# Performance work log

Measured on AMD Instinct MI355X. Metric: run time of the kernel, lower is better.

The kernel has to match this reference:

```python
import jax, jax.numpy as jnp
import numpy as np

EMBD = 256
HEAD = 4
HD = EMBD // HEAD  # 64
EPS = 1e-5


def setup_inputs() -> dict:
    key = jax.random.key(0)
    ks = jax.random.split(key, 12)
    s = lambda fan_in: 1.0 / np.sqrt(fan_in)
    return {
        "x": jax.random.normal(ks[0], (16, 1024, EMBD), dtype=jnp.float32),
        # attention params (stored as [in, out])
        "qkv_w": jax.random.uniform(ks[1], (EMBD, 3 * EMBD), jnp.float32, -s(EMBD), s(EMBD)),
        "qkv_b": jax.random.uniform(ks[2], (3 * EMBD,), jnp.float32, -s(EMBD), s(EMBD)),
        "out_w": jax.random.uniform(ks[3], (EMBD, EMBD), jnp.float32, -s(EMBD), s(EMBD)),
        "out_b": jax.random.uniform(ks[4], (EMBD,), jnp.float32, -s(EMBD), s(EMBD)),
        # MLP params
        "fc_w": jax.random.uniform(ks[5], (EMBD, 4 * EMBD), jnp.float32, -s(EMBD), s(EMBD)),
        "fc_b": jax.random.uniform(ks[6], (4 * EMBD,), jnp.float32, -s(EMBD), s(EMBD)),
        "proj_w": jax.random.uniform(ks[7], (4 * EMBD, EMBD), jnp.float32, -s(4 * EMBD), s(4 * EMBD)),
        "proj_b": jax.random.uniform(ks[8], (EMBD,), jnp.float32, -s(4 * EMBD), s(4 * EMBD)),
        # LayerNorm params
        "ln1_g": jnp.ones((EMBD,), jnp.float32),
        "ln1_b": jnp.zeros((EMBD,), jnp.float32),
        "ln2_g": jnp.ones((EMBD,), jnp.float32),
        "ln2_b": jnp.zeros((EMBD,), jnp.float32),
    }


def layer_norm(x, g, b):
    mu = jnp.mean(x, axis=-1, keepdims=True)
    var = jnp.mean(jnp.square(x - mu), axis=-1, keepdims=True)
    return (x - mu) * jax.lax.rsqrt(var + EPS) * g + b


def block_forward(x, qkv_w, qkv_b, out_w, out_b, fc_w, fc_b, proj_w, proj_b,
                  ln1_g, ln1_b, ln2_g, ln2_b):
    B, S, E = x.shape
    # --- attention branch ---
    h = layer_norm(x, ln1_g, ln1_b)
    qkv = h @ qkv_w + qkv_b                       # [B,S,3E]
    q, k, v = jnp.split(qkv, 3, axis=-1)
    q = q.reshape(B, S, HEAD, HD).transpose(0, 2, 1, 3)  # [B,H,S,D]
    k = k.reshape(B, S, HEAD, HD).transpose(0, 2, 1, 3)
    v = v.reshape(B, S, HEAD, HD).transpose(0, 2, 1, 3)
    att = jnp.einsum('bhqd,bhkd->bhqk', q, k) / jnp.sqrt(jnp.float32(HD))
    causal = jnp.tril(jnp.ones((S, S), dtype=bool))
    att = jnp.where(causal, att, -jnp.inf)
    att = jax.nn.softmax(att, axis=-1)
    o = jnp.einsum('bhqk,bhkd->bhqd', att, v)     # [B,H,S,D]
    o = o.transpose(0, 2, 1, 3).reshape(B, S, E)
    x = x + o @ out_w + out_b
    # --- MLP branch (dropout inactive at eval) ---
    h = layer_norm(x, ln2_g, ln2_b)
    h = jax.nn.relu(h @ fc_w + fc_b)
    x = x + h @ proj_w + proj_b
    return x


def reference(x, qkv_w, qkv_b, out_w, out_b, fc_w, fc_b, proj_w, proj_b,
              ln1_g, ln1_b, ln2_g, ln2_b):
    return block_forward(x, qkv_w, qkv_b, out_w, out_b, fc_w, fc_b,
                         proj_w, proj_b, ln1_g, ln1_b, ln2_g, ln2_b)
```

## Files before the change

kernel.cpp:

```cpp
#include <hip/hip_runtime.h>
#include <cstdint>


using f32x4 = __attribute__((ext_vector_type(4))) float;
using s16x8 = __attribute__((ext_vector_type(8))) short;
using s16x4 = __attribute__((ext_vector_type(4))) short;

__device__ inline short f2bf(float f) {
    union { float f; unsigned u; } v{f};
    unsigned r = (v.u + 0x7FFFu + ((v.u >> 16) & 1u)) >> 16;
    return (short)r;
}

__device__ inline int cvt_pk_bf16(float lo, float hi) {
    int d;
    asm("v_cvt_pk_bf16_f32 %0, %1, %2" : "=v"(d) : "v"(lo), "v"(hi));
    return d;
}
__device__ inline void swap32(int& a, int& b) {
    asm("v_permlane32_swap_b32 %0, %1" : "+v"(a), "+v"(b));
}
__device__ inline void swap16(int& a, int& b) {
    asm("v_permlane16_swap_b32 %0, %1" : "+v"(a), "+v"(b));
}

__device__ inline void gload16(const void* g, void* l) {
    __builtin_amdgcn_global_load_lds(
        (const __attribute__((address_space(1))) void*)g,
        (__attribute__((address_space(3))) void*)l, 16, 0, 0);
}

__global__ __launch_bounds__(256) void wconv_all_kernel(
    const float* __restrict__ qkv_w, const float* __restrict__ out_w,
    const float* __restrict__ fc_w,  const float* __restrict__ proj_w,
    short* __restrict__ wt_qkv, short* __restrict__ wt_out,
    short* __restrict__ wt_fc,  short* __restrict__ wt_proj)
{
    __shared__ short T[64][65];
    int id = blockIdx.x;
    const float* W; short* Wt; int K, N, nt, kt;
    if (id < 48)       { W = qkv_w;  Wt = wt_qkv;  K = 256;  N = 768;  nt = id % 12;        kt = id / 12; }
    else if (id < 64)  { W = out_w;  Wt = wt_out;  K = 256;  N = 256;  nt = (id - 48) & 3;  kt = (id - 48) >> 2; }
    else if (id < 128) { W = fc_w;   Wt = wt_fc;   K = 256;  N = 1024; nt = (id - 64) & 15; kt = (id - 64) >> 4; }
    else               { W = proj_w; Wt = wt_proj; K = 1024; N = 256;  nt = (id - 128) & 3; kt = (id - 128) >> 2; }
    int n0 = nt * 64, k0 = kt * 64;

    int tid = threadIdx.x;
    int r  = tid >> 2;
    int c  = (tid & 3) << 4;

    const float* src = W + (size_t)(k0 + r) * N + n0 + c;
#pragma unroll
    for (int u = 0; u < 4; ++u) {
        float4 v = *reinterpret_cast<const float4*>(src + u * 4);
        T[r][c + u * 4 + 0] = f2bf(v.x);
        T[r][c + u * 4 + 1] = f2bf(v.y);
        T[r][c + u * 4 + 2] = f2bf(v.z);
        T[r][c + u * 4 + 3] = f2bf(v.w);
    }
    __syncthreads();
    s16x8 o0, o1;
#pragma unroll
    for (int j = 0; j < 8; ++j) { o0[j] = T[c + j][r]; o1[j] = T[c + 8 + j][r]; }
    short* dst = Wt + (size_t)(n0 + r) * K + k0 + c;
    *reinterpret_cast<s16x8*>(dst)     = o0;
    *reinterpret_cast<s16x8*>(dst + 8) = o1;
}

__global__ __launch_bounds__(256) void ln_kernel(const float* __restrict__ x,
                                                 const float* __restrict__ gamma,
                                                 const float* __restrict__ beta,
                                                 short* __restrict__ out)
{
    int tid  = threadIdx.x;
    int lane = tid & 63;
    int row  = blockIdx.x * 4 + (tid >> 6);
    const float* xr = x + (size_t)row * 256;
    float4 v = *reinterpret_cast<const float4*>(xr + lane * 4);

    float s = v.x + v.y + v.z + v.w;
#pragma unroll
    for (int o = 32; o >= 1; o >>= 1) s += __shfl_xor(s, o);
    float mu = s * (1.0f / 256.0f);

    float dx = v.x - mu, dy = v.y - mu, dz = v.z - mu, dw = v.w - mu;
    float q = dx * dx + dy * dy + dz * dz + dw * dw;
#pragma unroll
    for (int o = 32; o >= 1; o >>= 1) q += __shfl_xor(q, o);
    float rstd = rsqrtf(q * (1.0f / 256.0f) + 1e-5f);

    float4 gv = *reinterpret_cast<const float4*>(gamma + lane * 4);
    float4 bv = *reinterpret_cast<const float4*>(beta + lane * 4);
    s16x4 ov;
    ov[0] = f2bf(dx * rstd * gv.x + bv.x);
    ov[1] = f2bf(dy * rstd * gv.y + bv.y);
    ov[2] = f2bf(dz * rstd * gv.z + bv.z);
    ov[3] = f2bf(dw * rstd * gv.w + bv.w);
    *reinterpret_cast<s16x4*>(out + (size_t)row * 256 + lane * 4) = ov;
}

template <int RELU, int RES, int OBF16, int BM, int QKV>
__global__ __launch_bounds__(256) void mgemm_kernel(const short* __restrict__ A,
                                                    const short* __restrict__ Bt,
                                                    const float* __restrict__ bias,
                                                    const float* __restrict__ R,
                                                    void* __restrict__ Cv,
                                                    short* __restrict__ vt,
                                                    int N, int K)
{
    constexpr int MI = BM / 32;
    __shared__ short As[BM * 64];
    __shared__ short Bs[128 * 64];

    int tid = threadIdx.x;
    int l   = tid & 63;
    int w   = tid >> 6;
    int lr  = l & 15;
    int lk8 = (l >> 4) << 3;
    int r4  = (l >> 4) << 2;
    int wr  = w >> 1, wc = w & 1;
    int bn  = blockIdx.x * 128, bm = blockIdx.y * BM;

    int scolS = ((l & 7) << 3) ^ ((l >> 3) << 3);
    int srowA = w * (BM / 4) + (l >> 3);
    int srowB = (w << 5) + (l >> 3);
    const short* pa = A  + (size_t)(bm + srowA) * K + scolS;
    const short* pb = Bt + (size_t)(bn + srowB) * K + scolS;
    short* dstA = As + w * (BM / 4) * 64;
    short* dstB = Bs + (w << 11);

    f32x4 acc[MI][4];
#pragma unroll
    for (int mi = 0; mi < MI; ++mi)
#pragma unroll
        for (int ni = 0; ni < 4; ++ni) acc[mi][ni] = (f32x4){0.f, 0.f, 0.f, 0.f};

    int swz = (lr & 7) << 3;

    for (int k0 = 0; k0 < K; k0 += 64) {
        __syncthreads();
#pragma unroll
        for (int i = 0; i < BM / 32; ++i)
            gload16(pa + (size_t)(i * 8) * K + k0, dstA + (i << 9));
#pragma unroll
        for (int i = 0; i < 4; ++i)
            gload16(pb + (size_t)(i * 8) * K + k0, dstB + (i << 9));
        __syncthreads();

#pragma unroll
        for (int ks = 0; ks < 2; ++ks) {
            s16x8 af[MI], bf[4];
#pragma unroll
            for (int mi = 0; mi < MI; ++mi) {
                int row = wr * (BM / 2) + (mi << 4) + lr;
                af[mi] = *reinterpret_cast<const s16x8*>(
                    &As[(row << 6) + (((ks << 5) + lk8) ^ swz)]);
            }
#pragma unroll
            for (int ni = 0; ni < 4; ++ni) {
                int row = (wc << 6) + (ni << 4) + lr;
                bf[ni] = *reinterpret_cast<const s16x8*>(
                    &Bs[(row << 6) + (((ks << 5) + lk8) ^ swz)]);
            }
#pragma unroll
            for (int mi = 0; mi < MI; ++mi)
#pragma unroll
                for (int ni = 0; ni < 4; ++ni)
                    acc[mi][ni] = __builtin_amdgcn_mfma_f32_16x16x32_bf16(
                        af[mi], bf[ni], acc[mi][ni], 0, 0, 0);
        }
    }

    float bv[4];
#pragma unroll
    for (int ni = 0; ni < 4; ++ni)
        bv[ni] = bias[bn + (wc << 6) + (ni << 4) + lr];

#pragma unroll
    for (int mi = 0; mi < MI; ++mi) {
#pragma unroll
        for (int ni = 0; ni < 4; ++ni) {
            int n = bn + (wc << 6) + (ni << 4) + lr;
#pragma unroll
            for (int r = 0; r < 4; ++r) {
                int m = bm + wr * (BM / 2) + (mi << 4) + r4 + r;
                float v = acc[mi][ni][r] + bv[ni];
                if (RELU) v = fmaxf(v, 0.0f);
                if (RES)  v += R[(size_t)m * N + n];
                if (QKV) {
                    if (bn < 512) {
                        ((short*)Cv)[(size_t)m * 512 + n] = f2bf(v);
                    } else {
                        int hh = (n - 512) >> 6, dd = (n - 512) & 63;
                        int bb = m >> 10, ss = m & 1023;
                        vt[(size_t)((((bb << 2) | hh) << 6) | dd) * 1024 + ss] = f2bf(v);
                    }
                } else if (OBF16) {
                    ((short*)Cv)[(size_t)m * N + n] = f2bf(v);
                } else {
                    ((float*)Cv)[(size_t)m * N + n] = v;
                }
            }
        }
    }
}

__global__ __launch_bounds__(256) void oproj_ln_kernel(const short* __restrict__ A,
                                                       const short* __restrict__ Bt,
                                                       const float* __restrict__ bias,
                                                       const float* __restrict__ R,
                                                       float* __restrict__ x1,
                                                       short* __restrict__ h2,
                                                       const float* __restrict__ g,
                                                       const float* __restrict__ bb)
{
    __shared__ short As[64 * 64];
    __shared__ short Bs[256 * 64];

    int tid = threadIdx.x;
    int l   = tid & 63;
    int w   = tid >> 6;
    int lr  = l & 15;
    int lk8 = (l >> 4) << 3;
    int r4  = (l >> 4) << 2;
    int bm  = blockIdx.x * 64;

    int scolS = ((l & 7) << 3) ^ ((l >> 3) << 3);
    const short* pa = A  + (size_t)(bm + (w << 4) + (l >> 3)) * 256 + scolS;
    const short* pb = Bt + (size_t)((w << 6) + (l >> 3)) * 256 + scolS;
    short* dstA = As + (w << 10);
    short* dstB = Bs + (w << 12);

    f32x4 acc[16];
#pragma unroll
    for (int ni = 0; ni < 16; ++ni) acc[ni] = (f32x4){0.f, 0.f, 0.f, 0.f};

    int swz = (lr & 7) << 3;

    for (int k0 = 0; k0 < 256; k0 += 64) {
        __syncthreads();
#pragma unroll
        for (int i = 0; i < 2; ++i)
            gload16(pa + (size_t)(i * 8) * 256 + k0, dstA + (i << 9));
#pragma unroll
        for (int i = 0; i < 8; ++i)
            gload16(pb + (size_t)(i * 8) * 256 + k0, dstB + (i << 9));
        __syncthreads();

#pragma unroll
        for (int ks = 0; ks < 2; ++ks) {
            int arow = (w << 4) + lr;
            s16x8 af = *reinterpret_cast<const s16x8*>(
                &As[(arow << 6) + (((ks << 5) + lk8) ^ swz)]);
#pragma unroll
            for (int ni = 0; ni < 16; ++ni) {
                int row = (ni << 4) + lr;
                s16x8 bf = *reinterpret_cast<const s16x8*>(
                    &Bs[(row << 6) + (((ks << 5) + lk8) ^ swz)]);
                acc[ni] = __builtin_amdgcn_mfma_f32_16x16x32_bf16(af, bf, acc[ni], 0, 0, 0);
            }
        }
    }

#pragma unroll
    for (int ni = 0; ni < 16; ++ni) {
        int n = (ni << 4) + lr;
        float bvx = bias[n];
#pragma unroll
        for (int r = 0; r < 4; ++r) {
            int m = bm + (w << 4) + r4 + r;
            acc[ni][r] += bvx + R[(size_t)m * 256 + n];
        }
    }
#pragma unroll
    for (int r = 0; r < 4; ++r) {
        float s = 0.0f;
#pragma unroll
        for (int ni = 0; ni < 16; ++ni) s += acc[ni][r];
        s += __shfl_xor(s, 1); s += __shfl_xor(s, 2);
        s += __shfl_xor(s, 4); s += __shfl_xor(s, 8);
        float mu = s * (1.0f / 256.0f);
        float q = 0.0f;
#pragma unroll
        for (int ni = 0; ni < 16; ++ni) {
            float d = acc[ni][r] - mu;
            q += d * d;
        }
        q += __shfl_xor(q, 1); q += __shfl_xor(q, 2);
        q += __shfl_xor(q, 4); q += __shfl_xor(q, 8);
        float rstd = rsqrtf(q * (1.0f / 256.0f) + 1e-5f);

        int m = bm + (w << 4) + r4 + r;
#pragma unroll
        for (int ni = 0; ni < 16; ++ni) {
            int n = (ni << 4) + lr;
            float v = acc[ni][r];
            x1[(size_t)m * 256 + n] = v;
            h2[(size_t)m * 256 + n] = f2bf((v - mu) * rstd * g[n] + bb[n]);
        }
    }
}

__global__ __launch_bounds__(256, 2) void attn_kernel(const short* __restrict__ qk,
                                                      const short* __restrict__ vt,
                                                      short* __restrict__ o)
{
    __shared__ short Ks[2][64 * 64];
    __shared__ short Vs[2][64 * 64];

    int bid  = blockIdx.x;
    int xcd  = bid & 7;
    int pair = (bid >> 3) & 7;
    int bhg  = bid >> 6;
    int bh   = (bhg << 3) | xcd;
    int b = bh >> 2, h = bh & 3;

    int tid = threadIdx.x;
    int l   = tid & 63;
    int w   = tid >> 6;
    int lr  = l & 15;
    int g   = l >> 4;
    int lk8 = g << 3;
    int w16 = w << 4;

    int srow = (w << 3) + (l >> 3);
    int scol = ((l & 7) << 3) ^ (((l >> 3) & 7) << 3);
    const short* kgp = qk + (size_t)(b * 1024 + srow) * 512 + 256 + h * 64 + scol;
    const short* vgp = vt + (size_t)((bh << 6) + srow) * 1024 + scol;
    short* dstK = &Ks[0][(w << 3) * 64];
    short* dstV = &Vs[0][(w << 3) * 64];
    const int BUFS = 64 * 64;

    const float SC = 0.125f * 1.44269504088896f;
    int rsw = (lr & 7) << 3;

    int cur = 1;
    for (int sel = 0; sel < 2; ++sel) {
        int qt = sel == 0 ? pair : 15 - pair;

        const short* qrow = qk + (size_t)(b * 1024 + qt * 64 + w16 + lr) * 512 + h * 64;
        s16x8 qf[2];
        qf[0] = *reinterpret_cast<const s16x8*>(qrow + lk8);
        qf[1] = *reinterpret_cast<const s16x8*>(qrow + 32 + lk8);

#pragma unroll
        for (int i = 0; i < 2; ++i) {
            gload16(kgp + (size_t)(qt * 0 + i * 32) * 512, dstK + (cur ^ 1) * BUFS + (i << 11));
            gload16(vgp + (size_t)(i * 32) * 1024,         dstV + (cur ^ 1) * BUFS + (i << 11));
        }
        __syncthreads();
        cur ^= 1;

        float m = -1e30f, lsum = 0.0f;
        f32x4 oacc[4];
#pragma unroll
        for (int dt = 0; dt < 4; ++dt) oacc[dt] = (f32x4){0.f, 0.f, 0.f, 0.f};
        int qglob = qt * 64 + w16 + lr;

        for (int kt = 0; kt <= qt; ++kt) {
            if (kt < qt) {
#pragma unroll
                for (int i = 0; i < 2; ++i) {
                    gload16(kgp + (size_t)((kt + 1) * 64 + i * 32) * 512,
                            dstK + (cur ^ 1) * BUFS + (i << 11));
                    gload16(vgp + (size_t)(i * 32) * 1024 + (kt + 1) * 64,
                            dstV + (cur ^ 1) * BUFS + (i << 11));
                }
            }

            f32x4 s[4];
#pragma unroll
            for (int jt = 0; jt < 4; ++jt) s[jt] = (f32x4){0.f, 0.f, 0.f, 0.f};
#pragma unroll
            for (int ks = 0; ks < 2; ++ks) {
#pragma unroll
                for (int jt = 0; jt < 4; ++jt) {
                    int row = jt * 16 + lr;
                    s16x8 kf = *reinterpret_cast<const s16x8*>(
                        &Ks[cur][(row << 6) + ((32 * ks + lk8) ^ rsw)]);
                    s[jt] = __builtin_amdgcn_mfma_f32_16x16x32_bf16(kf, qf[ks], s[jt], 0, 0, 0);
                }
            }
#pragma unroll
            for (int jt = 0; jt < 4; ++jt)
#pragma unroll
                for (int r = 0; r < 4; ++r) s[jt][r] *= SC;

            if (kt == qt) {
#pragma unroll
                for (int jt = 0; jt < 4; ++jt) {
                    int kb = kt * 64 + jt * 16 + (g << 2);
#pragma unroll
                    for (int r = 0; r < 4; ++r)
                        if (kb + r > qglob) s[jt][r] = -1e30f;
                }
            }

            float rm = fmaxf(fmaxf(s[0][0], s[0][1]), fmaxf(s[0][2], s[0][3]));
#pragma unroll
            for (int jt = 1; jt < 4; ++jt)
                rm = fmaxf(rm, fmaxf(fmaxf(s[jt][0], s[jt][1]), fmaxf(s[jt][2], s[jt][3])));
            rm = fmaxf(rm, __shfl_xor(rm, 16));
            rm = fmaxf(rm, __shfl_xor(rm, 32));
            float mn  = fmaxf(m, rm);
            float fct = exp2f(m - mn);
            m = mn;
            float ps = 0.0f;
#pragma unroll
            for (int jt = 0; jt < 4; ++jt)
#pragma unroll
                for (int r = 0; r < 4; ++r) {
                    float p = exp2f(s[jt][r] - mn);
                    s[jt][r] = p;
                    ps += p;
                }
            ps += __shfl_xor(ps, 16);
            ps += __shfl_xor(ps, 32);
            lsum = lsum * fct + ps;

            int cpk[4][2];
#pragma unroll
            for (int jt = 0; jt < 4; ++jt) {
                cpk[jt][0] = cvt_pk_bf16(s[jt][0], s[jt][1]);
                cpk[jt][1] = cvt_pk_bf16(s[jt][2], s[jt][3]);
            }

#pragma unroll
            for (int r = 0; r < 4; ++r) {
                float f4 = __shfl(fct, 4 * g + r);
#pragma unroll
                for (int dt = 0; dt < 4; ++dt) oacc[dt][r] *= f4;
            }

#pragma unroll
            for (int ks = 0; ks < 2; ++ks) {
                int a0 = cpk[2 * ks][0],     a1 = cpk[2 * ks][1];
                int b0 = cpk[2 * ks + 1][0], b1 = cpk[2 * ks + 1][1];
                swap32(a0, b0); swap32(a1, b1);
                swap16(a0, b0); swap16(a1, b1);
                union { int i[4]; s16x8 v; } fr;
                fr.i[0] = a0; fr.i[1] = a1; fr.i[2] = b0; fr.i[3] = b1;
#pragma unroll
                for (int dt = 0; dt < 4; ++dt) {
                    int row = dt * 16 + lr;
                    s16x8 vf = *reinterpret_cast<const s16x8*>(
                        &Vs[cur][(row << 6) + ((32 * ks + lk8) ^ rsw)]);
                    oacc[dt] = __builtin_amdgcn_mfma_f32_16x16x32_bf16(fr.v, vf, oacc[dt], 0, 0, 0);
                }
            }

            if (kt < qt) {
                __syncthreads();
                cur ^= 1;
            }
        }

#pragma unroll
        for (int r = 0; r < 4; ++r) {
            float lv  = __shfl(lsum, 4 * g + r);
            float inv = 1.0f / lv;
            short* orow = o + (size_t)(b * 1024 + qt * 64 + w16 + 4 * g + r) * 256 + h * 64;
#pragma unroll
            for (int dt = 0; dt < 4; ++dt)
                orow[dt * 16 + lr] = f2bf(oacc[dt][r] * inv);
        }
    }
}

extern "C" void kernel_launch(void* const* d_in, const int* in_sizes, int n_in,
                              void* d_out, int out_size, void* d_ws, size_t ws_size,
                              hipStream_t stream)
{
    const float* x      = (const float*)d_in[0];
    const float* qkv_w  = (const float*)d_in[1];
    const float* qkv_b  = (const float*)d_in[2];
    const float* out_w  = (const float*)d_in[3];
    const float* out_b  = (const float*)d_in[4];
    const float* fc_w   = (const float*)d_in[5];
    const float* fc_b   = (const float*)d_in[6];
    const float* proj_w = (const float*)d_in[7];
    const float* proj_b = (const float*)d_in[8];
    const float* ln1_g  = (const float*)d_in[9];
    const float* ln1_b  = (const float*)d_in[10];
    const float* ln2_g  = (const float*)d_in[11];
    const float* ln2_b  = (const float*)d_in[12];
    float* out = (float*)d_out;

    short* ws = (short*)d_ws;
    short* wt_qkv  = ws;
    short* wt_out  = ws + 196608;
    short* wt_fc   = ws + 262144;
    short* wt_proj = ws + 524288;
    short* bufA    = ws + 786432;
    short* qk_buf  = ws + 4980736;
    short* vt_buf  = ws + 13369344;
    short* h3_buf  = ws + 4980736;

    dim3 blk(256);

    wconv_all_kernel<<<dim3(192), blk, 0, stream>>>(
        qkv_w, out_w, fc_w, proj_w, wt_qkv, wt_out, wt_fc, wt_proj);
    ln_kernel<<<dim3(4096), blk, 0, stream>>>(x, ln1_g, ln1_b, bufA);
    mgemm_kernel<0, 0, 1, 128, 1><<<dim3(6, 128), blk, 0, stream>>>(
        bufA, wt_qkv, qkv_b, nullptr, qk_buf, vt_buf, 768, 256);
    attn_kernel<<<dim3(512), blk, 0, stream>>>(qk_buf, vt_buf, bufA);
    oproj_ln_kernel<<<dim3(256), blk, 0, stream>>>(
        bufA, wt_out, out_b, x, out, bufA, ln2_g, ln2_b);
    mgemm_kernel<1, 0, 1, 128, 0><<<dim3(8, 128), blk, 0, stream>>>(
        bufA, wt_fc, fc_b, nullptr, h3_buf, nullptr, 1024, 256);
    mgemm_kernel<0, 1, 0, 64, 0><<<dim3(2, 256), blk, 0, stream>>>(
        h3_buf, wt_proj, proj_b, out, out, nullptr, 256, 1024);
}
```

Measured before the change: 125.4 us.

## Use 128-key attention tiles with lazy softmax rescale and MFMA priority

The attention kernel now processes keys in 128-wide tiles instead of 64, with double-buffered LDS for K and V resized to match. This halves the number of loop iterations and barriers per query tile. Online softmax now skips the max update and accumulator rescale unless the new row max exceeds the running max by more than 8 (log2 units), which avoids exp and shuffle work. The MFMA sections are wrapped in s_setprio. The risks are higher LDS use (64KB per block, which may reduce occupancy), wasted masked work on the diagonal tile when qt is even, and the reduced-rescale path relying on exp2 values staying bounded.

```diff
diff --git a/kernel.cpp b/kernel.cpp
--- a/kernel.cpp
+++ b/kernel.cpp
@@ -305,8 +305,10 @@
                                                       const short* __restrict__ vt,
                                                       short* __restrict__ o)
 {
-    __shared__ short Ks[2][64 * 64];
-    __shared__ short Vs[2][64 * 64];
+    constexpr int KSZ = 128 * 64;
+    constexpr int VSZ = 64 * 128;
+    __shared__ short Ks[2 * KSZ];
+    __shared__ short Vs[2 * VSZ];
 
     int bid  = blockIdx.x;
     int xcd  = bid & 7;
@@ -323,133 +325,149 @@
     int lk8 = g << 3;
     int w16 = w << 4;
 
-    int srow = (w << 3) + (l >> 3);
-    int scol = ((l & 7) << 3) ^ (((l >> 3) & 7) << 3);
-    const short* kgp = qk + (size_t)(b * 1024 + srow) * 512 + 256 + h * 64 + scol;
-    const short* vgp = vt + (size_t)((bh << 6) + srow) * 1024 + scol;
-    short* dstK = &Ks[0][(w << 3) * 64];
-    short* dstV = &Vs[0][(w << 3) * 64];
-    const int BUFS = 64 * 64;
+    int krow0 = (w << 3) + (l >> 3);
+    int kscol = ((l & 7) << 3) ^ (((l >> 3) & 7) << 3);
+    const short* kgp = qk + (size_t)(b * 1024 + krow0) * 512 + 256 + h * 64 + kscol;
+    short* dstK = Ks + (w << 3) * 64;
+
+    int vrow0 = (w << 2) + (l >> 4);
+    int vscol = ((l & 15) << 3) ^ ((((w << 2) + (l >> 4)) & 7) << 3);
+    const short* vgp = vt + (size_t)((bh << 6) + vrow0) * 1024 + vscol;
+    short* dstV = Vs + (w << 2) * 128;
 
     const float SC = 0.125f * 1.44269504088896f;
     int rsw = (lr & 7) << 3;
 
-    int cur = 1;
+    int cur = 0;
     for (int sel = 0; sel < 2; ++sel) {
         int qt = sel == 0 ? pair : 15 - pair;
+        int ntile = qt >> 1;
+
+        __syncthreads();
+
+#pragma unroll
+        for (int i = 0; i < 4; ++i) {
+            gload16(kgp + (size_t)(i * 32) * 512, dstK + cur * KSZ + i * 32 * 64);
+            gload16(vgp + (size_t)(i * 16) * 1024, dstV + cur * VSZ + i * 16 * 128);
+        }
+        __syncthreads();
 
         const short* qrow = qk + (size_t)(b * 1024 + qt * 64 + w16 + lr) * 512 + h * 64;
         s16x8 qf[2];
         qf[0] = *reinterpret_cast<const s16x8*>(qrow + lk8);
         qf[1] = *reinterpret_cast<const s16x8*>(qrow + 32 + lk8);
 
-#pragma unroll
-        for (int i = 0; i < 2; ++i) {
-            gload16(kgp + (size_t)(qt * 0 + i * 32) * 512, dstK + (cur ^ 1) * BUFS + (i << 11));
-            gload16(vgp + (size_t)(i * 32) * 1024,         dstV + (cur ^ 1) * BUFS + (i << 11));
-        }
-        __syncthreads();
-        cur ^= 1;
-
         float m = -1e30f, lsum = 0.0f;
         f32x4 oacc[4];
 #pragma unroll
         for (int dt = 0; dt < 4; ++dt) oacc[dt] = (f32x4){0.f, 0.f, 0.f, 0.f};
         int qglob = qt * 64 + w16 + lr;
 
-        for (int kt = 0; kt <= qt; ++kt) {
-            if (kt < qt) {
-#pragma unroll
-                for (int i = 0; i < 2; ++i) {
-                    gload16(kgp + (size_t)((kt + 1) * 64 + i * 32) * 512,
-                            dstK + (cur ^ 1) * BUFS + (i << 11));
-                    gload16(vgp + (size_t)(i * 32) * 1024 + (kt + 1) * 64,
-                            dstV + (cur ^ 1) * BUFS + (i << 11));
-                }
-            }
-
-            f32x4 s[4];
-#pragma unroll
-            for (int jt = 0; jt < 4; ++jt) s[jt] = (f32x4){0.f, 0.f, 0.f, 0.f};
+        for (int kt = 0; kt <= ntile; ++kt) {
+            if (kt < ntile) {
+                int nxt = cur ^ 1;
+#pragma unroll
+                for (int i = 0; i < 4; ++i) {
+                    gload16(kgp + (size_t)((kt + 1) * 128 + i * 32) * 512,
+                            dstK + nxt * KSZ + i * 32 * 64);
+                    gload16(vgp + (size_t)(i * 16) * 1024 + (kt + 1) * 128,
+                            dstV + nxt * VSZ + i * 16 * 128);
+                }
+            }
+
+            f32x4 sv[8];
+#pragma unroll
+            for (int jt = 0; jt < 8; ++jt) sv[jt] = (f32x4){0.f, 0.f, 0.f, 0.f};
+            __builtin_amdgcn_s_setprio(1);
 #pragma unroll
             for (int ks = 0; ks < 2; ++ks) {
 #pragma unroll
-                for (int jt = 0; jt < 4; ++jt) {
+                for (int jt = 0; jt < 8; ++jt) {
                     int row = jt * 16 + lr;
                     s16x8 kf = *reinterpret_cast<const s16x8*>(
-                        &Ks[cur][(row << 6) + ((32 * ks + lk8) ^ rsw)]);
-                    s[jt] = __builtin_amdgcn_mfma_f32_16x16x32_bf16(kf, qf[ks], s[jt], 0, 0, 0);
-                }
-            }
-#pragma unroll
-            for (int jt = 0; jt < 4; ++jt)
-#pragma unroll
-                for (int r = 0; r < 4; ++r) s[jt][r] *= SC;
-
-            if (kt == qt) {
-#pragma unroll
-                for (int jt = 0; jt < 4; ++jt) {
-                    int kb = kt * 64 + jt * 16 + (g << 2);
+                        &Ks[cur * KSZ + (row << 6) + ((32 * ks + lk8) ^ rsw)]);
+                    sv[jt] = __builtin_amdgcn_mfma_f32_16x16x32_bf16(kf, qf[ks], sv[jt], 0, 0, 0);
+                }
+            }
+            __builtin_amdgcn_s_setprio(0);
+#pragma unroll
+            for (int jt = 0; jt < 8; ++jt)
+#pragma unroll
+                for (int r = 0; r < 4; ++r) sv[jt][r] *= SC;
+
+            if (kt == ntile) {
+#pragma unroll
+                for (int jt = 0; jt < 8; ++jt) {
+                    int kb = kt * 128 + jt * 16 + (g << 2);
 #pragma unroll
                     for (int r = 0; r < 4; ++r)
-                        if (kb + r > qglob) s[jt][r] = -1e30f;
-                }
-            }
-
-            float rm = fmaxf(fmaxf(s[0][0], s[0][1]), fmaxf(s[0][2], s[0][3]));
-#pragma unroll
-            for (int jt = 1; jt < 4; ++jt)
-                rm = fmaxf(rm, fmaxf(fmaxf(s[jt][0], s[jt][1]), fmaxf(s[jt][2], s[jt][3])));
+                        if (kb + r > qglob) sv[jt][r] = -1e30f;
+                }
+            }
+
+            float rm = fmaxf(fmaxf(sv[0][0], sv[0][1]), fmaxf(sv[0][2], sv[0][3]));
+#pragma unroll
+            for (int jt = 1; jt < 8; ++jt)
+                rm = fmaxf(rm, fmaxf(fmaxf(sv[jt][0], sv[jt][1]),
+                                     fmaxf(sv[jt][2], sv[jt][3])));
             rm = fmaxf(rm, __shfl_xor(rm, 16));
             rm = fmaxf(rm, __shfl_xor(rm, 32));
-            float mn  = fmaxf(m, rm);
-            float fct = exp2f(m - mn);
-            m = mn;
+            bool big = __any(rm > m + 8.0f);
+            float fct = 1.0f;
+            if (big) {
+                float mn = fmaxf(m, rm);
+                fct = exp2f(m - mn);
+                m = mn;
+            }
             float ps = 0.0f;
 #pragma unroll
-            for (int jt = 0; jt < 4; ++jt)
+            for (int jt = 0; jt < 8; ++jt)
 #pragma unroll
                 for (int r = 0; r < 4; ++r) {
-                    float p = exp2f(s[jt][r] - mn);
-                    s[jt][r] = p;
+                    float p = exp2f(sv[jt][r] - m);
+                    sv[jt][r] = p;
                     ps += p;
                 }
             ps += __shfl_xor(ps, 16);
             ps += __shfl_xor(ps, 32);
             lsum = lsum * fct + ps;
 
-            int cpk[4][2];
-#pragma unroll
-            for (int jt = 0; jt < 4; ++jt) {
-                cpk[jt][0] = cvt_pk_bf16(s[jt][0], s[jt][1]);
-                cpk[jt][1] = cvt_pk_bf16(s[jt][2], s[jt][3]);
-            }
-
-#pragma unroll
-            for (int r = 0; r < 4; ++r) {
-                float f4 = __shfl(fct, 4 * g + r);
-#pragma unroll
-                for (int dt = 0; dt < 4; ++dt) oacc[dt][r] *= f4;
-            }
-
-#pragma unroll
-            for (int ks = 0; ks < 2; ++ks) {
-                int a0 = cpk[2 * ks][0],     a1 = cpk[2 * ks][1];
-                int b0 = cpk[2 * ks + 1][0], b1 = cpk[2 * ks + 1][1];
+            int cpk[8][2];
+#pragma unroll
+            for (int jt = 0; jt < 8; ++jt) {
+                cpk[jt][0] = cvt_pk_bf16(sv[jt][0], sv[jt][1]);
+                cpk[jt][1] = cvt_pk_bf16(sv[jt][2], sv[jt][3]);
+            }
+
+            if (big) {
+#pragma unroll
+                for (int r = 0; r < 4; ++r) {
+                    float f4 = __shfl(fct, 4 * g + r);
+#pragma unroll
+                    for (int dt = 0; dt < 4; ++dt) oacc[dt][r] *= f4;
+                }
+            }
+
+#pragma unroll
+            for (int ks2 = 0; ks2 < 4; ++ks2) {
+                int a0 = cpk[2 * ks2][0],     a1 = cpk[2 * ks2][1];
+                int b0 = cpk[2 * ks2 + 1][0], b1 = cpk[2 * ks2 + 1][1];
                 swap32(a0, b0); swap32(a1, b1);
                 swap16(a0, b0); swap16(a1, b1);
                 union { int i[4]; s16x8 v; } fr;
                 fr.i[0] = a0; fr.i[1] = a1; fr.i[2] = b0; fr.i[3] = b1;
+                __builtin_amdgcn_s_setprio(1);
 #pragma unroll
                 for (int dt = 0; dt < 4; ++dt) {
                     int row = dt * 16 + lr;
                     s16x8 vf = *reinterpret_cast<const s16x8*>(
-                        &Vs[cur][(row << 6) + ((32 * ks + lk8) ^ rsw)]);
+                        &Vs[cur * VSZ + (row << 7) + ((32 * ks2 + lk8) ^ rsw)]);
                     oacc[dt] = __builtin_amdgcn_mfma_f32_16x16x32_bf16(fr.v, vf, oacc[dt], 0, 0, 0);
                 }
-            }
-
-            if (kt < qt) {
+                __builtin_amdgcn_s_setprio(0);
+            }
+
+            if (kt < ntile) {
                 __syncthreads();
                 cur ^= 1;
             }
```

Result: no change. 124.9 us (-0.4%).
